# Optimization experiments

Hardware: AMD Instinct MI355X
Metric: run time of the kernel (lower is better)

Reference implementation:

```python
import jax, jax.numpy as jnp
import numpy as np

SEQLEN = (512, 1024, 2048, 1536, 768, 1280, 896, 640)
HEAD_NUM = 16
HIDDEN = 1024  # head_size = 64


def setup_inputs() -> dict:
    key = jax.random.key(0)
    k1, k2 = jax.random.split(key)
    total_a = HEAD_NUM * sum(s * s for s in SEQLEN)  # packed per-seq (H, s, s) blocks
    a = jax.random.normal(k1, (total_a,), dtype=jnp.float32) * 0.02
    b = jax.random.normal(k2, (sum(SEQLEN), HIDDEN), dtype=jnp.float32)
    return {"a": a, "b": b, "seqlen": list(SEQLEN), "head_num": HEAD_NUM}


def reference(a, b, seqlen, head_num):
    """Ragged strided bmm2: per sequence i, per head h:
    C_i[:, h*hs:(h+1)*hs] = A_i[h] @ B_i[:, h*hs:(h+1)*hs].
    a packed flat as sum_i (head_num, s_i, s_i); b is (sum(s), hidden).
    """
    hidden = b.shape[1]
    hs = hidden // head_num
    outs = []
    a_off = 0
    t_off = 0
    for s in seqlen:  # static loop over ragged batch (lengths are compile-time)
        ai = jax.lax.dynamic_slice(a, (a_off,), (head_num * s * s,)).reshape(head_num, s, s)
        bi = jax.lax.dynamic_slice(b, (t_off, 0), (s, hidden)).reshape(s, head_num, hs)
        # (H, q, k) x (k, H, d) -> (q, H, d) -> (q, hidden)
        ci = jnp.einsum('hqk,khd->qhd', ai, bi).reshape(s, hidden)
        outs.append(ci)
        a_off += head_num * s * s
        t_off += s
    return jnp.concatenate(outs, axis=0)  # (sum(seqlen), hidden)
```

## Files before the change

kernel.cpp:

```cpp
#include <hip/hip_runtime.h>
#include <hip/hip_bf16.h>

typedef __attribute__((ext_vector_type(4))) float f32x4;
typedef __attribute__((ext_vector_type(8))) short bf16x8;
typedef __attribute__((ext_vector_type(4))) short bf16x4;

__device__ __forceinline__ unsigned cvt2(float lo, float hi) {
    float2 t; t.x = lo; t.y = hi;
    __hip_bfloat162 h = __float22bfloat162_rn(t);
    union { __hip_bfloat162 h; unsigned u; } c; c.h = h; return c.u;
}

__global__ __launch_bounds__(256, 3) void bmm2_k(const float* __restrict__ a,
                                                 const float* __restrict__ b,
                                                 float* __restrict__ out) {
    const int  cumblk[9] = {0,256,448,608,736,848,944,1024,1088};
    const int  slen[8]   = {2048,1536,1280,1024,896,768,640,512};
    const long aoff[8]   = {20971520,88080384,135266304,4194304,161480704,125829120,174325760,0};
    const int  toff[8]   = {1536,3584,5888,512,7168,5120,8064,0};

    __shared__ unsigned short As[128 * 72];
    __shared__ unsigned short Bs[64 * 72];

    int bid = blockIdx.x;
    int i = 0;
    #pragma unroll
    for (int t = 0; t < 7; ++t) if (bid >= cumblk[t + 1]) i = t + 1;
    int rem  = bid - cumblk[i];
    int s    = slen[i];
    int nmb  = s >> 7;
    int head = rem / nmb;
    int mb   = rem - head * nmb;

    const float* A  = a + aoff[i] + (long)head * s * s + (long)mb * 128 * s;
    const float* Bp = b + (long)toff[i] * 1024 + head * 64;
    float*       Cp = out + (long)(toff[i] + mb * 128) * 1024 + head * 64;

    int tid = threadIdx.x, lane = tid & 63, wave = tid >> 6;
    int lrow = lane & 15, lgrp = lane >> 4;

    int arow = tid >> 4;
    int kf   = (tid & 15) * 4;
    const float* Ast = A + (long)arow * s + kf;

    int bj0 = (tid & 15) * 4;
    int bk0 = (tid >> 4) * 4;
    const float* Bst = Bp + (long)bk0 * 1024 + bj0;

    f32x4 rA[8], rB[4];
    f32x4 acc[2][4] = {};
    int NT = s >> 6;

    #pragma unroll
    for (int q = 0; q < 8; ++q) rA[q] = *(const f32x4*)(Ast + (long)(q * 16) * s);
    #pragma unroll
    for (int q = 0; q < 4; ++q) rB[q] = *(const f32x4*)(Bst + (long)q * 1024);

    for (int t = 0; t < NT; ++t) {
        __syncthreads();

        #pragma unroll
        for (int q = 0; q < 8; ++q) {
            int r = q * 16 + arow;
            union { bf16x4 v; unsigned u[2]; } w;
            w.u[0] = cvt2(rA[q][0], rA[q][1]);
            w.u[1] = cvt2(rA[q][2], rA[q][3]);
            *(bf16x4*)&As[r * 72 + kf] = w.v;
        }
        #pragma unroll
        for (int e = 0; e < 4; ++e) {
            union { bf16x4 v; unsigned u[2]; } w;
            w.u[0] = cvt2(rB[0][e], rB[1][e]);
            w.u[1] = cvt2(rB[2][e], rB[3][e]);
            *(bf16x4*)&Bs[(bj0 + e) * 72 + bk0] = w.v;
        }

        __syncthreads();

        if (t + 1 < NT) {
            int kn = (t + 1) << 6;
            #pragma unroll
            for (int q = 0; q < 8; ++q) rA[q] = *(const f32x4*)(Ast + (long)(q * 16) * s + kn);
            #pragma unroll
            for (int q = 0; q < 4; ++q) rB[q] = *(const f32x4*)(Bst + (long)(kn + q) * 1024);
        }

        #pragma unroll
        for (int ks = 0; ks < 2; ++ks) {
            bf16x8 af0 = *(const bf16x8*)&As[(wave * 32 + lrow) * 72 + ks * 32 + lgrp * 8];
            bf16x8 af1 = *(const bf16x8*)&As[(wave * 32 + 16 + lrow) * 72 + ks * 32 + lgrp * 8];
            bf16x8 bf[4];
            #pragma unroll
            for (int n = 0; n < 4; ++n)
                bf[n] = *(const bf16x8*)&Bs[(n * 16 + lrow) * 72 + ks * 32 + lgrp * 8];
            #pragma unroll
            for (int n = 0; n < 4; ++n) {
                acc[0][n] = __builtin_amdgcn_mfma_f32_16x16x32_bf16(af0, bf[n], acc[0][n], 0, 0, 0);
                acc[1][n] = __builtin_amdgcn_mfma_f32_16x16x32_bf16(af1, bf[n], acc[1][n], 0, 0, 0);
            }
        }
    }

    #pragma unroll
    for (int mt = 0; mt < 2; ++mt)
        #pragma unroll
        for (int n = 0; n < 4; ++n)
            #pragma unroll
            for (int r = 0; r < 4; ++r) {
                int q = wave * 32 + mt * 16 + lgrp * 4 + r;
                Cp[(long)q * 1024 + n * 16 + lrow] = acc[mt][n][r];
            }
}

extern "C" void kernel_launch(void* const* d_in, const int* in_sizes, int n_in,
                              void* d_out, int out_size, void* d_ws, size_t ws_size,
                              hipStream_t stream) {
    const float* a = (const float*)d_in[0];
    const float* b = (const float*)d_in[1];
    float* out = (float*)d_out;
    bmm2_k<<<1088, 256, 0, stream>>>(a, b, out);
}
```

Measured before the change: 178.1 us.

## Halve M-tile to 64 rows, double-buffer LDS with two-stage register prefetch

Shrinks each block's row tile from 128 to 64, doubling the grid to 2176 blocks and raising occupancy hints to 4 blocks per CU. The K loop is restructured into two alternating LDS buffers with two register prefetch stages, so global loads run two tiles ahead of compute, using raw s_barrier plus explicit waitcnt. A loads and C stores become nontemporal. The intent is better latency hiding and more parallelism for this memory-bound kernel, at the cost of re-reading the B tile twice as often.

```diff
diff --git a/kernel.cpp b/kernel.cpp
--- a/kernel.cpp
+++ b/kernel.cpp
@@ -11,16 +11,16 @@
     union { __hip_bfloat162 h; unsigned u; } c; c.h = h; return c.u;
 }
 
-__global__ __launch_bounds__(256, 3) void bmm2_k(const float* __restrict__ a,
+__global__ __launch_bounds__(256, 4) void bmm2_k(const float* __restrict__ a,
                                                  const float* __restrict__ b,
                                                  float* __restrict__ out) {
-    const int  cumblk[9] = {0,256,448,608,736,848,944,1024,1088};
+    const int  cumblk[9] = {0,512,896,1216,1472,1696,1888,2048,2176};
     const int  slen[8]   = {2048,1536,1280,1024,896,768,640,512};
     const long aoff[8]   = {20971520,88080384,135266304,4194304,161480704,125829120,174325760,0};
     const int  toff[8]   = {1536,3584,5888,512,7168,5120,8064,0};
 
-    __shared__ unsigned short As[128 * 72];
-    __shared__ unsigned short Bs[64 * 72];
+    __shared__ unsigned short As[2][64 * 72];
+    __shared__ unsigned short Bs[2][64 * 72];
 
     int bid = blockIdx.x;
     int i = 0;
@@ -28,88 +28,117 @@
     for (int t = 0; t < 7; ++t) if (bid >= cumblk[t + 1]) i = t + 1;
     int rem  = bid - cumblk[i];
     int s    = slen[i];
-    int nmb  = s >> 7;
+    int nmb  = s >> 6;
     int head = rem / nmb;
     int mb   = rem - head * nmb;
 
-    const float* A  = a + aoff[i] + (long)head * s * s + (long)mb * 128 * s;
+    const float* A  = a + aoff[i] + (long)head * s * s + (long)mb * 64 * s;
     const float* Bp = b + (long)toff[i] * 1024 + head * 64;
-    float*       Cp = out + (long)(toff[i] + mb * 128) * 1024 + head * 64;
+    float*       Cp = out + (long)(toff[i] + mb * 64) * 1024 + head * 64;
 
     int tid = threadIdx.x, lane = tid & 63, wave = tid >> 6;
     int lrow = lane & 15, lgrp = lane >> 4;
 
     int arow = tid >> 4;
-    int kf   = (tid & 15) * 4;
-    const float* Ast = A + (long)arow * s + kf;
+    int kq   = tid & 15;
+    const float* Ast = A + (long)arow * s + kq * 4;
 
-    int bj0 = (tid & 15) * 4;
-    int bk0 = (tid >> 4) * 4;
-    const float* Bst = Bp + (long)bk0 * 1024 + bj0;
+    int bcol = (tid & 15) * 4;
+    int btok = (tid >> 4) * 4;
+    const float* Bst = Bp + (long)btok * 1024 + bcol;
 
-    f32x4 rA[8], rB[4];
-    f32x4 acc[2][4] = {};
-    int NT = s >> 6;
+    f32x4 lA0[4], lB0[4], lA1[4], lB1[4];
+    f32x4 acc[4] = {};
 
     #pragma unroll
-    for (int q = 0; q < 8; ++q) rA[q] = *(const f32x4*)(Ast + (long)(q * 16) * s);
-    #pragma unroll
-    for (int q = 0; q < 4; ++q) rB[q] = *(const f32x4*)(Bst + (long)q * 1024);
+    for (int q = 0; q < 4; ++q) {
+        lA0[q] = __builtin_nontemporal_load((const f32x4*)(Ast + (long)(16 * q) * s));
+        lA1[q] = __builtin_nontemporal_load((const f32x4*)(Ast + (long)(16 * q) * s + 64));
+        lB0[q] = *(const f32x4*)(Bst + (long)q * 1024);
+        lB1[q] = *(const f32x4*)(Bst + (long)(64 + q) * 1024);
+    }
 
-    for (int t = 0; t < NT; ++t) {
-        __syncthreads();
-
+    int NTt = s >> 6;
+    for (int t = 0; t < NTt; t += 2) {
+        __builtin_amdgcn_s_barrier();
         #pragma unroll
-        for (int q = 0; q < 8; ++q) {
-            int r = q * 16 + arow;
+        for (int q = 0; q < 4; ++q) {
             union { bf16x4 v; unsigned u[2]; } w;
-            w.u[0] = cvt2(rA[q][0], rA[q][1]);
-            w.u[1] = cvt2(rA[q][2], rA[q][3]);
-            *(bf16x4*)&As[r * 72 + kf] = w.v;
+            w.u[0] = cvt2(lA0[q][0], lA0[q][1]);
+            w.u[1] = cvt2(lA0[q][2], lA0[q][3]);
+            *(bf16x4*)&As[0][(arow + 16 * q) * 72 + kq * 4] = w.v;
         }
         #pragma unroll
         for (int e = 0; e < 4; ++e) {
             union { bf16x4 v; unsigned u[2]; } w;
-            w.u[0] = cvt2(rB[0][e], rB[1][e]);
-            w.u[1] = cvt2(rB[2][e], rB[3][e]);
-            *(bf16x4*)&Bs[(bj0 + e) * 72 + bk0] = w.v;
+            w.u[0] = cvt2(lB0[0][e], lB0[1][e]);
+            w.u[1] = cvt2(lB0[2][e], lB0[3][e]);
+            *(bf16x4*)&Bs[0][(bcol + e) * 72 + btok] = w.v;
         }
-
-        __syncthreads();
-
-        if (t + 1 < NT) {
-            int kn = (t + 1) << 6;
+        {
+            long kn = (t + 2 < NTt) ? ((long)(t + 2) << 6) : 0;
             #pragma unroll
-            for (int q = 0; q < 8; ++q) rA[q] = *(const f32x4*)(Ast + (long)(q * 16) * s + kn);
-            #pragma unroll
-            for (int q = 0; q < 4; ++q) rB[q] = *(const f32x4*)(Bst + (long)(kn + q) * 1024);
+            for (int q = 0; q < 4; ++q) {
+                lA0[q] = __builtin_nontemporal_load((const f32x4*)(Ast + (long)(16 * q) * s + kn));
+                lB0[q] = *(const f32x4*)(Bst + (kn + q) * 1024);
+            }
         }
-
+        asm volatile("s_waitcnt lgkmcnt(0)" ::: "memory");
+        __builtin_amdgcn_sched_barrier(0);
+        __builtin_amdgcn_s_barrier();
         #pragma unroll
         for (int ks = 0; ks < 2; ++ks) {
-            bf16x8 af0 = *(const bf16x8*)&As[(wave * 32 + lrow) * 72 + ks * 32 + lgrp * 8];
-            bf16x8 af1 = *(const bf16x8*)&As[(wave * 32 + 16 + lrow) * 72 + ks * 32 + lgrp * 8];
-            bf16x8 bf[4];
-            #pragma unroll
-            for (int n = 0; n < 4; ++n)
-                bf[n] = *(const bf16x8*)&Bs[(n * 16 + lrow) * 72 + ks * 32 + lgrp * 8];
+            bf16x8 af = *(const bf16x8*)&As[0][(wave * 16 + lrow) * 72 + ks * 32 + lgrp * 8];
             #pragma unroll
             for (int n = 0; n < 4; ++n) {
-                acc[0][n] = __builtin_amdgcn_mfma_f32_16x16x32_bf16(af0, bf[n], acc[0][n], 0, 0, 0);
-                acc[1][n] = __builtin_amdgcn_mfma_f32_16x16x32_bf16(af1, bf[n], acc[1][n], 0, 0, 0);
+                bf16x8 bf = *(const bf16x8*)&Bs[0][(n * 16 + lrow) * 72 + ks * 32 + lgrp * 8];
+                acc[n] = __builtin_amdgcn_mfma_f32_16x16x32_bf16(af, bf, acc[n], 0, 0, 0);
+            }
+        }
+        __builtin_amdgcn_s_barrier();
+        #pragma unroll
+        for (int q = 0; q < 4; ++q) {
+            union { bf16x4 v; unsigned u[2]; } w;
+            w.u[0] = cvt2(lA1[q][0], lA1[q][1]);
+            w.u[1] = cvt2(lA1[q][2], lA1[q][3]);
+            *(bf16x4*)&As[1][(arow + 16 * q) * 72 + kq * 4] = w.v;
+        }
+        #pragma unroll
+        for (int e = 0; e < 4; ++e) {
+            union { bf16x4 v; unsigned u[2]; } w;
+            w.u[0] = cvt2(lB1[0][e], lB1[1][e]);
+            w.u[1] = cvt2(lB1[2][e], lB1[3][e]);
+            *(bf16x4*)&Bs[1][(bcol + e) * 72 + btok] = w.v;
+        }
+        {
+            long kn = (t + 3 < NTt) ? ((long)(t + 3) << 6) : 0;
+            #pragma unroll
+            for (int q = 0; q < 4; ++q) {
+                lA1[q] = __builtin_nontemporal_load((const f32x4*)(Ast + (long)(16 * q) * s + kn));
+                lB1[q] = *(const f32x4*)(Bst + (kn + q) * 1024);
+            }
+        }
+        asm volatile("s_waitcnt lgkmcnt(0)" ::: "memory");
+        __builtin_amdgcn_sched_barrier(0);
+        __builtin_amdgcn_s_barrier();
+        #pragma unroll
+        for (int ks = 0; ks < 2; ++ks) {
+            bf16x8 af = *(const bf16x8*)&As[1][(wave * 16 + lrow) * 72 + ks * 32 + lgrp * 8];
+            #pragma unroll
+            for (int n = 0; n < 4; ++n) {
+                bf16x8 bf = *(const bf16x8*)&Bs[1][(n * 16 + lrow) * 72 + ks * 32 + lgrp * 8];
+                acc[n] = __builtin_amdgcn_mfma_f32_16x16x32_bf16(af, bf, acc[n], 0, 0, 0);
             }
         }
     }
 
     #pragma unroll
-    for (int mt = 0; mt < 2; ++mt)
+    for (int n = 0; n < 4; ++n)
         #pragma unroll
-        for (int n = 0; n < 4; ++n)
-            #pragma unroll
-            for (int r = 0; r < 4; ++r) {
-                int q = wave * 32 + mt * 16 + lgrp * 4 + r;
-                Cp[(long)q * 1024 + n * 16 + lrow] = acc[mt][n][r];
-            }
+        for (int r = 0; r < 4; ++r) {
+            int q = wave * 16 + lgrp * 4 + r;
+            __builtin_nontemporal_store(acc[n][r], &Cp[(long)q * 1024 + n * 16 + lrow]);
+        }
 }
 
 extern "C" void kernel_launch(void* const* d_in, const int* in_sizes, int n_in,
@@ -118,5 +147,5 @@
     const float* a = (const float*)d_in[0];
     const float* b = (const float*)d_in[1];
     float* out = (float*)d_out;
-    bmm2_k<<<1088, 256, 0, stream>>>(a, b, out);
+    bmm2_k<<<2176, 256, 0, stream>>>(a, b, out);
 }
```

After: 173.3 us, median of 2. 2.7% less time.

## Shrink M tile to 32 rows, deepen K step to 256 with nontemporal streaming

Applied to the files above, without the earlier changes.

Each block now computes a 32-row output tile over a 256-wide K slice per iteration instead of 128 rows over 64, quadrupling the grid. Each thread keeps many more global loads in flight, and A loads and C stores are marked nontemporal to stream the large A matrix. The cost is B being reloaded by four times as many blocks and larger register and LDS footprints, plus clamped tail handling for partial K slices.

```diff
diff --git a/kernel.cpp b/kernel.cpp
--- a/kernel.cpp
+++ b/kernel.cpp
@@ -5,22 +5,29 @@
 typedef __attribute__((ext_vector_type(8))) short bf16x8;
 typedef __attribute__((ext_vector_type(4))) short bf16x4;
 
+#define LDK 264
+
 __device__ __forceinline__ unsigned cvt2(float lo, float hi) {
     float2 t; t.x = lo; t.y = hi;
     __hip_bfloat162 h = __float22bfloat162_rn(t);
     union { __hip_bfloat162 h; unsigned u; } c; c.h = h; return c.u;
 }
+__device__ __forceinline__ bf16x4 pk4(float a0, float a1, float a2, float a3) {
+    union { bf16x4 v; unsigned u[2]; } w;
+    w.u[0] = cvt2(a0, a1); w.u[1] = cvt2(a2, a3);
+    return w.v;
+}
 
 __global__ __launch_bounds__(256, 3) void bmm2_k(const float* __restrict__ a,
                                                  const float* __restrict__ b,
                                                  float* __restrict__ out) {
-    const int  cumblk[9] = {0,256,448,608,736,848,944,1024,1088};
+    const int  cumblk[9] = {0,1024,1792,2432,2944,3392,3776,4096,4352};
     const int  slen[8]   = {2048,1536,1280,1024,896,768,640,512};
     const long aoff[8]   = {20971520,88080384,135266304,4194304,161480704,125829120,174325760,0};
     const int  toff[8]   = {1536,3584,5888,512,7168,5120,8064,0};
 
-    __shared__ unsigned short As[128 * 72];
-    __shared__ unsigned short Bs[64 * 72];
+    __shared__ unsigned short As[32 * LDK];
+    __shared__ unsigned short Bs[64 * LDK];
 
     int bid = blockIdx.x;
     int i = 0;
@@ -28,88 +35,90 @@
     for (int t = 0; t < 7; ++t) if (bid >= cumblk[t + 1]) i = t + 1;
     int rem  = bid - cumblk[i];
     int s    = slen[i];
-    int nmb  = s >> 7;
+    int nmb  = s >> 5;
     int head = rem / nmb;
     int mb   = rem - head * nmb;
 
-    const float* A  = a + aoff[i] + (long)head * s * s + (long)mb * 128 * s;
+    const float* A  = a + aoff[i] + (long)head * s * s + (long)mb * 32 * s;
     const float* Bp = b + (long)toff[i] * 1024 + head * 64;
-    float*       Cp = out + (long)(toff[i] + mb * 128) * 1024 + head * 64;
+    float*       Cp = out + (long)(toff[i] + mb * 32) * 1024 + head * 64;
 
     int tid = threadIdx.x, lane = tid & 63, wave = tid >> 6;
     int lrow = lane & 15, lgrp = lane >> 4;
 
-    int arow = tid >> 4;
-    int kf   = (tid & 15) * 4;
-    const float* Ast = A + (long)arow * s + kf;
+    int arow = tid >> 3, ac = (tid & 7) * 4;
+    const float* Arow = A + (long)arow * s;
+    int bc = (tid & 15) * 4, tb = (tid >> 4) * 16;
 
-    int bj0 = (tid & 15) * 4;
-    int bk0 = (tid >> 4) * 4;
-    const float* Bst = Bp + (long)bk0 * 1024 + bj0;
+    f32x4 rA[8], rB[16];
+    f32x4 acc0 = {}, acc1 = {};
 
-    f32x4 rA[8], rB[4];
-    f32x4 acc[2][4] = {};
-    int NT = s >> 6;
+    int NP = (s + 255) >> 8;
 
-    #pragma unroll
-    for (int q = 0; q < 8; ++q) rA[q] = *(const f32x4*)(Ast + (long)(q * 16) * s);
-    #pragma unroll
-    for (int q = 0; q < 4; ++q) rB[q] = *(const f32x4*)(Bst + (long)q * 1024);
+    auto issue = [&](long kn, bool full) {
+        if (full) {
+            #pragma unroll
+            for (int q = 0; q < 8; ++q)
+                rA[q] = __builtin_nontemporal_load((const f32x4*)(Arow + kn + ac + q * 32));
+            #pragma unroll
+            for (int q = 0; q < 16; ++q)
+                rB[q] = *(const f32x4*)(Bp + (kn + tb + q) * 1024 + bc);
+        } else {
+            #pragma unroll
+            for (int q = 0; q < 8; ++q) {
+                long k = kn + ac + q * 32;
+                long kc = (k < (long)s - 4) ? k : (long)s - 4;
+                f32x4 v = __builtin_nontemporal_load((const f32x4*)(Arow + kc));
+                if (k >= (long)s) v = (f32x4){0.f, 0.f, 0.f, 0.f};
+                rA[q] = v;
+            }
+            #pragma unroll
+            for (int q = 0; q < 16; ++q) {
+                long tk = kn + tb + q;
+                if (tk > (long)s - 1) tk = (long)s - 1;
+                rB[q] = *(const f32x4*)(Bp + tk * 1024 + bc);
+            }
+        }
+    };
 
-    for (int t = 0; t < NT; ++t) {
-        __syncthreads();
+    issue(0, true);
+
+    for (int p = 0; p < NP; ++p) {
+        __builtin_amdgcn_s_barrier();
 
         #pragma unroll
-        for (int q = 0; q < 8; ++q) {
-            int r = q * 16 + arow;
-            union { bf16x4 v; unsigned u[2]; } w;
-            w.u[0] = cvt2(rA[q][0], rA[q][1]);
-            w.u[1] = cvt2(rA[q][2], rA[q][3]);
-            *(bf16x4*)&As[r * 72 + kf] = w.v;
-        }
+        for (int q = 0; q < 8; ++q)
+            *(bf16x4*)&As[arow * LDK + ac + q * 32] = pk4(rA[q][0], rA[q][1], rA[q][2], rA[q][3]);
         #pragma unroll
-        for (int e = 0; e < 4; ++e) {
-            union { bf16x4 v; unsigned u[2]; } w;
-            w.u[0] = cvt2(rB[0][e], rB[1][e]);
-            w.u[1] = cvt2(rB[2][e], rB[3][e]);
-            *(bf16x4*)&Bs[(bj0 + e) * 72 + bk0] = w.v;
-        }
+        for (int g = 0; g < 4; ++g)
+            #pragma unroll
+            for (int e = 0; e < 4; ++e)
+                *(bf16x4*)&Bs[(bc + e) * LDK + tb + g * 4] =
+                    pk4(rB[g*4][e], rB[g*4+1][e], rB[g*4+2][e], rB[g*4+3][e]);
 
-        __syncthreads();
+        long kn = (p + 1 < NP) ? ((long)(p + 1) << 8) : 0;
+        issue(kn, kn + 256 <= (long)s);
 
-        if (t + 1 < NT) {
-            int kn = (t + 1) << 6;
-            #pragma unroll
-            for (int q = 0; q < 8; ++q) rA[q] = *(const f32x4*)(Ast + (long)(q * 16) * s + kn);
-            #pragma unroll
-            for (int q = 0; q < 4; ++q) rB[q] = *(const f32x4*)(Bst + (long)(kn + q) * 1024);
-        }
+        asm volatile("s_waitcnt lgkmcnt(0)" ::: "memory");
+        __builtin_amdgcn_sched_barrier(0);
+        __builtin_amdgcn_s_barrier();
 
         #pragma unroll
-        for (int ks = 0; ks < 2; ++ks) {
-            bf16x8 af0 = *(const bf16x8*)&As[(wave * 32 + lrow) * 72 + ks * 32 + lgrp * 8];
-            bf16x8 af1 = *(const bf16x8*)&As[(wave * 32 + 16 + lrow) * 72 + ks * 32 + lgrp * 8];
-            bf16x8 bf[4];
-            #pragma unroll
-            for (int n = 0; n < 4; ++n)
-                bf[n] = *(const bf16x8*)&Bs[(n * 16 + lrow) * 72 + ks * 32 + lgrp * 8];
-            #pragma unroll
-            for (int n = 0; n < 4; ++n) {
-                acc[0][n] = __builtin_amdgcn_mfma_f32_16x16x32_bf16(af0, bf[n], acc[0][n], 0, 0, 0);
-                acc[1][n] = __builtin_amdgcn_mfma_f32_16x16x32_bf16(af1, bf[n], acc[1][n], 0, 0, 0);
-            }
+        for (int ks = 0; ks < 8; ++ks) {
+            bf16x8 bf  = *(const bf16x8*)&Bs[(wave * 16 + lrow) * LDK + ks * 32 + lgrp * 8];
+            bf16x8 af0 = *(const bf16x8*)&As[lrow * LDK + ks * 32 + lgrp * 8];
+            bf16x8 af1 = *(const bf16x8*)&As[(16 + lrow) * LDK + ks * 32 + lgrp * 8];
+            acc0 = __builtin_amdgcn_mfma_f32_16x16x32_bf16(af0, bf, acc0, 0, 0, 0);
+            acc1 = __builtin_amdgcn_mfma_f32_16x16x32_bf16(af1, bf, acc1, 0, 0, 0);
         }
     }
 
     #pragma unroll
-    for (int mt = 0; mt < 2; ++mt)
-        #pragma unroll
-        for (int n = 0; n < 4; ++n)
-            #pragma unroll
-            for (int r = 0; r < 4; ++r) {
-                int q = wave * 32 + mt * 16 + lgrp * 4 + r;
-                Cp[(long)q * 1024 + n * 16 + lrow] = acc[mt][n][r];
-            }
+    for (int r = 0; r < 4; ++r) {
+        int q0 = lgrp * 4 + r;
+        __builtin_nontemporal_store(acc0[r], &Cp[(long)q0 * 1024 + wave * 16 + lrow]);
+        __builtin_nontemporal_store(acc1[r], &Cp[(long)(16 + q0) * 1024 + wave * 16 + lrow]);
+    }
 }
 
 extern "C" void kernel_launch(void* const* d_in, const int* in_sizes, int n_in,
@@ -118,5 +127,5 @@
     const float* a = (const float*)d_in[0];
     const float* b = (const float*)d_in[1];
     float* out = (float*)d_out;
-    bmm2_k<<<1088, 256, 0, stream>>>(a, b, out);
+    bmm2_k<<<4352, 256, 0, stream>>>(a, b, out);
 }
```

New measurement: 205.0 us. 15.1% more time.
